# Optimization experiments

Hardware: AMD Instinct MI355X
Metric: run time of the kernel (lower is better)

Reference implementation:

```python
import jax, jax.numpy as jnp
import numpy as np

B, F, H, W = 1, 6, 20, 26
S = F * H * W            # 3120 tokens
DIM, NH, HD = 1536, 12, 128
C = HD // 2              # 64 rotary channels
T_C = C - 2 * (C // 3)   # 22 temporal channels
H_C = C // 3             # 21
W_C = C // 3             # 21
LOCAL_FRAMES = 4         # local_attn_size (in frames)
SINK_FRAMES = 1          # sink_size (in frames)
EPS = 1e-6
MAX_POS = 1024


def _angle_table(n_ch):
    inv = 1.0 / (10000.0 ** (np.arange(n_ch, dtype=np.float64) / n_ch))
    return np.outer(np.arange(MAX_POS, dtype=np.float64), inv)


def setup_inputs() -> dict:
    key = jax.random.key(0)
    ks = jax.random.split(key, 8)
    sc = 0.02
    ang = np.concatenate([_angle_table(T_C), _angle_table(H_C), _angle_table(W_C)], axis=1)  # [1024, 64]
    return {
        "x": jax.random.normal(ks[0], (B, S, DIM), jnp.float32),
        "seq_lens": jnp.array([S], jnp.int32),
        "grid_sizes": jnp.array([[F, H, W]], jnp.int32),
        "freqs_cos": jnp.asarray(np.cos(ang), jnp.float32),
        "freqs_sin": jnp.asarray(np.sin(ang), jnp.float32),
        "Wq": jax.random.normal(ks[1], (DIM, DIM), jnp.float32) * sc,
        "bq": jnp.zeros((DIM,), jnp.float32),
        "Wk": jax.random.normal(ks[2], (DIM, DIM), jnp.float32) * sc,
        "bk": jnp.zeros((DIM,), jnp.float32),
        "Wv": jax.random.normal(ks[3], (DIM, DIM), jnp.float32) * sc,
        "bv": jnp.zeros((DIM,), jnp.float32),
        "Wo": jax.random.normal(ks[4], (DIM, DIM), jnp.float32) * sc,
        "bo": jnp.zeros((DIM,), jnp.float32),
        "gq": jnp.ones((DIM,), jnp.float32),
        "gk": jnp.ones((DIM,), jnp.float32),
    }


def _rms_norm(x, g):
    # WanRMSNorm: x * rsqrt(mean(x^2) + eps) * weight
    return x * jax.lax.rsqrt(jnp.mean(x * x, axis=-1, keepdims=True) + EPS) * g


def _rope_apply(x, freqs_cos, freqs_sin):
    # x: [B, S, NH, HD]; per-token 3D (f,h,w) rotary on consecutive pairs.
    pos = jnp.arange(S)
    f = pos // (H * W)
    hh = (pos // W) % H
    ww = pos % W
    cos_t, cos_h, cos_w = freqs_cos[:, :T_C], freqs_cos[:, T_C:T_C + H_C], freqs_cos[:, T_C + H_C:]
    sin_t, sin_h, sin_w = freqs_sin[:, :T_C], freqs_sin[:, T_C:T_C + H_C], freqs_sin[:, T_C + H_C:]
    cos = jnp.concatenate([cos_t[f], cos_h[hh], cos_w[ww]], axis=-1)[None, :, None, :]  # [1,S,1,C]
    sin = jnp.concatenate([sin_t[f], sin_h[hh], sin_w[ww]], axis=-1)[None, :, None, :]
    xp = x.reshape(B, S, NH, C, 2)
    xr, xi = xp[..., 0], xp[..., 1]
    out = jnp.stack([xr * cos - xi * sin, xr * sin + xi * cos], axis=-1)
    return out.reshape(B, S, NH, HD)


def _block_mask():
    # frame-causal + local window (in frames) + sink frames: [S, S] bool
    fid = jnp.arange(S) // (H * W)
    fi, fj = fid[:, None], fid[None, :]
    return (fj <= fi) & ((fi - fj < LOCAL_FRAMES) | (fj < SINK_FRAMES))


def reference(x, seq_lens, grid_sizes, freqs_cos, freqs_sin,
              Wq, bq, Wk, bk, Wv, bv, Wo, bo, gq, gk):
    q = _rms_norm(x @ Wq + bq, gq).reshape(B, S, NH, HD)
    k = _rms_norm(x @ Wk + bk, gk).reshape(B, S, NH, HD)
    v = (x @ Wv + bv).reshape(B, S, NH, HD)
    rq = _rope_apply(q, freqs_cos, freqs_sin)
    rk = _rope_apply(k, freqs_cos, freqs_sin)
    scale = 1.0 / jnp.sqrt(jnp.asarray(HD, x.dtype))
    scores = jnp.einsum('bind,bjnd->bnij', rq, rk) * scale  # [B,NH,S,S]
    scores = jnp.where(_block_mask()[None, None], scores, jnp.finfo(scores.dtype).min)
    attn = jax.nn.softmax(scores, axis=-1)
    out = jnp.einsum('bnij,bjnd->bind', attn, v).reshape(B, S, DIM)
    return out @ Wo + bo
```

## Files before the change

kernel.cpp:

```cpp
#include <hip/hip_runtime.h>
#include <hip/hip_bf16.h>
#include <stdint.h>

typedef short v8s __attribute__((ext_vector_type(8)));
typedef float v4f __attribute__((ext_vector_type(4)));
typedef unsigned short u16;

#define S_LEN 3120
#define DIMN 1536
#define NHEAD 12
#define HDIM 128
#define FRM 520
#define NT64 49
#define T64_PH 166
#define TOT64 1992
#define NSTEP32 17
#define SCALE_QK 0.088388347648318447f
#define MAXOFF 12.0f

struct TaskMap {
  unsigned char tile[T64_PH];
  unsigned char frame[T64_PH];
  short accv[NT64];
  unsigned char nf[NT64];
};
constexpr TaskMap make_map() {
  TaskMap m{};
  int acc = 0;
  for (int tile = 0; tile < NT64; ++tile) {
    int q0t = tile * 64;
    int f_lo = q0t / FRM;
    int qhi = q0t + 63 < S_LEN - 1 ? q0t + 63 : S_LEN - 1;
    int f_hi = qhi / FRM;
    int fstart = f_lo - 3 > 0 ? f_lo - 3 : 0;
    int sink = fstart > 0 ? 1 : 0;
    int nf = f_hi - fstart + 1 + sink;
    m.accv[tile] = (short)acc;
    m.nf[tile] = (unsigned char)nf;
    for (int c = 0; c < nf; ++c) {
      m.tile[acc + c] = (unsigned char)tile;
      m.frame[acc + c] = (unsigned char)(sink ? (c == 0 ? 0 : fstart + c - 1) : (fstart + c));
    }
    acc += nf;
  }
  return m;
}
__device__ __constant__ TaskMap TM = make_map();

__device__ __forceinline__ v4f mfma16(v8s a, v8s b, v4f c) {
  return __builtin_amdgcn_mfma_f32_16x16x32_bf16(a, b, c, 0, 0, 0);
}
__device__ __forceinline__ float b2f(u16 u) {
  union { float f; unsigned int i; } x; x.i = ((unsigned int)u) << 16; return x.f;
}
__device__ __forceinline__ u16 f2b(float f) {
  union { float f; unsigned int i; } x; x.f = f;
  unsigned int r = x.i + 0x7FFFu + ((x.i >> 16) & 1u);
  return (u16)(r >> 16);
}
__device__ __forceinline__ void async16(const void* g, void* l) {
  __builtin_amdgcn_global_load_lds(
      (__attribute__((address_space(1))) const void*)g,
      (__attribute__((address_space(3))) void*)l, 16, 0, 0);
}

__global__ void detect_dtype(const u16* __restrict__ w, int* __restrict__ flag) {
  __shared__ int sh;
  int t = threadIdx.x;
  if (t == 0) sh = 0;
  __syncthreads();
  u16 m0 = (u16)(w[2 * t] & 0x7FFF);
  u16 m1 = (u16)(w[2 * t + 1] & 0x7FFF);
  if (m0 >= 0x4480 || m1 >= 0x4480) atomicOr(&sh, 1);
  __syncthreads();
  if (t == 0) *flag = sh;
}

struct PrepArgs {
  const void* tin[4]; u16* tout[4];
  const void* csrc[9]; u16* cdst[9]; int cn[9];
};
__global__ __launch_bounds__(256) void prep(PrepArgs a, const int* __restrict__ flag) {
  int isf = *flag;
  int z = blockIdx.z;
  int t = threadIdx.x;
  if (z < 4) {
    __shared__ u16 tile[32][33];
    const float* inf = (const float*)a.tin[z];
    const u16* inb = (const u16*)a.tin[z];
    u16* out = a.tout[z];
    int tx = t & 31, ty = t >> 5;
    int gr0 = blockIdx.y * 32, gc0 = blockIdx.x * 32;
#pragma unroll
    for (int i = 0; i < 4; ++i) {
      int r = ty + i * 8;
      size_t idx = (size_t)(gr0 + r) * DIMN + gc0 + tx;
      tile[r][tx] = isf ? f2b(inf[idx]) : inb[idx];
    }
    __syncthreads();
#pragma unroll
    for (int i = 0; i < 4; ++i) {
      int r = ty + i * 8;
      out[(size_t)(gc0 + r) * DIMN + gr0 + tx] = tile[tx][r];
    }
  } else {
    int id = z - 4;
    int n = a.cn[id];
    const float* sf = (const float*)a.csrc[id];
    const u16* sb = (const u16*)a.csrc[id];
    u16* d = a.cdst[id];
    int bidx = blockIdx.y * gridDim.x + blockIdx.x;
    int stride = gridDim.x * gridDim.y * 256;
    for (int i = bidx * 256 + t; i < n; i += stride)
      d[i] = isf ? f2b(sf[i]) : sb[i];
  }
}

__global__ __launch_bounds__(256) void transpose16(const u16* __restrict__ in,
                                                   u16* __restrict__ out,
                                                   int rows, int cols) {
  __shared__ u16 tile[32][33];
  int t = threadIdx.x;
  int tx = t & 31, ty = t >> 5;
  int gr0 = blockIdx.y * 32, gc0 = blockIdx.x * 32;
#pragma unroll
  for (int i = 0; i < 4; ++i) {
    int r = ty + i * 8;
    int gr = gr0 + r, gc = gc0 + tx;
    if (gr < rows && gc < cols) tile[r][tx] = in[(size_t)gr * cols + gc];
  }
  __syncthreads();
#pragma unroll
  for (int i = 0; i < 4; ++i) {
    int r = ty + i * 8;
    int orow = gc0 + r, ocol = gr0 + tx;
    if (orow < cols && ocol < rows) out[(size_t)orow * rows + ocol] = tile[tx][r];
  }
}

template <int MT, int NT>
__global__ __launch_bounds__(256) void gemm3(
    const u16* __restrict__ A,
    const u16* BT0, const u16* BT1, const u16* BT2,
    const u16* b0, const u16* b1, const u16* b2,
    void* C0, void* C1, void* C2, int M, const int* __restrict__ flag, int dyn) {
  static_assert(MT == 64, "4-wave layout assumes MT==64");
  const u16* BT; const u16* bias; void* C;
  if (blockIdx.z == 0)      { BT = BT0; bias = b0; C = C0; }
  else if (blockIdx.z == 1) { BT = BT1; bias = b1; C = C1; }
  else                      { BT = BT2; bias = b2; C = C2; }
  int f32out = dyn ? *flag : 0;
  __shared__ __align__(16) short As[MT * 64];
  __shared__ __align__(16) short Bs[NT * 64];
  int t = threadIdx.x, w = t >> 6, l = t & 63;
  int ln = l & 15, lg = l >> 4;
  int m0 = blockIdx.y * MT, n0 = blockIdx.x * NT;
  int lr = l >> 3;
  int gl = (l & 7) ^ lr;
  constexpr int ACH = MT / 32;
  constexpr int BCH = NT / 32;
  const u16* gAp[ACH]; short* lAp[ACH];
#pragma unroll
  for (int i = 0; i < ACH; ++i) {
    int c = w * ACH + i;
    int arow = min(m0 + c * 8 + lr, M - 1);
    gAp[i] = A + (size_t)arow * DIMN + gl * 8;
    lAp[i] = As + c * 512;
  }
  const u16* gBp[BCH]; short* lBp[BCH];
#pragma unroll
  for (int i = 0; i < BCH; ++i) {
    int c = w * BCH + i;
    int brow = n0 + c * 8 + lr;
    gBp[i] = BT + (size_t)brow * DIMN + gl * 8;
    lBp[i] = Bs + c * 512;
  }
  constexpr int NJ = NT / 64;
  int aoff[2][4], boff[2][NJ];
#pragma unroll
  for (int ks = 0; ks < 2; ++ks) {
#pragma unroll
    for (int i = 0; i < 4; ++i) {
      int ar = i * 16 + ln;
      aoff[ks][i] = ar * 64 + (((ks * 4 + lg) ^ (ar & 7)) * 8);
    }
#pragma unroll
    for (int j = 0; j < NJ; ++j) {
      int br = w * (NJ * 16) + j * 16 + ln;
      boff[ks][j] = br * 64 + (((ks * 4 + lg) ^ (br & 7)) * 8);
    }
  }
  v4f acc[4][NJ] = {};
  for (int k0 = 0; k0 < DIMN; k0 += 64) {
    __syncthreads();
#pragma unroll
    for (int i = 0; i < ACH; ++i) async16(gAp[i] + k0, lAp[i]);
#pragma unroll
    for (int i = 0; i < BCH; ++i) async16(gBp[i] + k0, lBp[i]);
    __syncthreads();
#pragma unroll
    for (int ks = 0; ks < 2; ++ks) {
      v8s af[4], bfr[NJ];
#pragma unroll
      for (int i = 0; i < 4; ++i) af[i] = *(const v8s*)(As + aoff[ks][i]);
#pragma unroll
      for (int j = 0; j < NJ; ++j) bfr[j] = *(const v8s*)(Bs + boff[ks][j]);
#pragma unroll
      for (int i = 0; i < 4; ++i)
#pragma unroll
        for (int j = 0; j < NJ; ++j) acc[i][j] = mfma16(af[i], bfr[j], acc[i][j]);
    }
  }
#pragma unroll
  for (int i = 0; i < 4; ++i) {
    int rb = m0 + i * 16 + lg * 4;
#pragma unroll
    for (int j = 0; j < NJ; ++j) {
      int col = n0 + w * (NJ * 16) + j * 16 + ln;
      float bv = b2f(bias[col]);
#pragma unroll
      for (int r = 0; r < 4; ++r) {
        int grow = rb + r;
        if (grow < M) {
          size_t idx = (size_t)grow * DIMN + col;
          float val = acc[i][j][r] + bv;
          if (f32out) ((float*)C)[idx] = val;
          else        ((u16*)C)[idx] = f2b(val);
        }
      }
    }
  }
}

__global__ __launch_bounds__(256) void norm_rope(u16* __restrict__ Q, u16* __restrict__ K,
                                                 const u16* __restrict__ gq,
                                                 const u16* __restrict__ gk,
                                                 const u16* __restrict__ fcos,
                                                 const u16* __restrict__ fsin) {
  int s = blockIdx.x;
  u16* base = (blockIdx.y == 0 ? Q : K) + (size_t)s * DIMN;
  const u16* g = (blockIdx.y == 0) ? gq : gk;
  int t = threadIdx.x;
  int e = t * 6;
  float x[6];
#pragma unroll
  for (int i = 0; i < 6; ++i) x[i] = b2f(base[e + i]);
  float ss = 0.f;
#pragma unroll
  for (int i = 0; i < 6; ++i) ss += x[i] * x[i];
#pragma unroll
  for (int off = 32; off > 0; off >>= 1) ss += __shfl_xor(ss, off);
  __shared__ float red[4];
  if ((t & 63) == 0) red[t >> 6] = ss;
  __syncthreads();
  float tot = red[0] + red[1] + red[2] + red[3];
  float rs = rsqrtf(tot * (1.0f / DIMN) + 1e-6f);
  int f = s / FRM;
  int hh = (s / 26) % 20;
  int ww = s % 26;
#pragma unroll
  for (int u = 0; u < 3; ++u) {
    int e0 = e + 2 * u;
    int c = (e0 & 127) >> 1;
    int p = (c < 22) ? f : ((c < 43) ? hh : ww);
    float co = b2f(fcos[p * 64 + c]);
    float si = b2f(fsin[p * 64 + c]);
    float xr = x[2 * u] * rs * b2f(g[e0]);
    float xi = x[2 * u + 1] * rs * b2f(g[e0 + 1]);
    base[e0]     = f2b(xr * co - xi * si);
    base[e0 + 1] = f2b(xr * si + xi * co);
  }
}

__global__ __launch_bounds__(128) void attn_block(const u16* __restrict__ Q,
                                                  const u16* __restrict__ K,
                                                  const u16* __restrict__ VT,
                                                  u16* __restrict__ Po,
                                                  float* __restrict__ Pl) {
  __shared__ __align__(16) short Ks[2][32 * 128];
  __shared__ __align__(16) short Vs[2][128 * 32];
  __shared__ __align__(16) short Pt[2][32 * 40];
  int t = threadIdx.x, w = t >> 6, l = t & 63;
  int ln = l & 15, lg = l >> 4;
  int task = blockIdx.x;
  int head = task / T64_PH, tid = task % T64_PH;
  int tile = TM.tile[tid], frame = TM.frame[tid];
  int q0 = tile * 64 + w * 32;
  v8s qf[2][4];
  bool rowok[2][4];
#pragma unroll
  for (int g = 0; g < 2; ++g) {
    int row = min(q0 + g * 16 + ln, S_LEN - 1);
    const u16* qp = Q + (size_t)row * DIMN + head * HDIM + lg * 8;
#pragma unroll
    for (int c = 0; c < 4; ++c) qf[g][c] = *(const v8s*)(qp + c * 32);
#pragma unroll
    for (int r = 0; r < 4; ++r) {
      int qr = q0 + g * 16 + lg * 4 + r;
      int fi = (qr < S_LEN) ? qr / FRM : -1;
      rowok[g][r] = (frame <= fi) && ((fi - frame) < 4 || frame == 0);
    }
  }
  float lsum[2][4] = {};
  v4f o[2][8] = {};
  int kbeg = frame * FRM, kend = kbeg + FRM;
  int kr_i[4], kgl_i[4], vd_i[4], vgl_i[4];
#pragma unroll
  for (int i = 0; i < 4; ++i) {
    int n = (w * 4 + i) * 64 + l;
    kr_i[i] = n >> 4;
    kgl_i[i] = (n & 15) ^ (kr_i[i] & 15);
    vd_i[i] = n >> 2;
    vgl_i[i] = (n & 3) ^ (vd_i[i] & 3);
  }
  const u16* Kb = K + head * HDIM;
  {
    int kb = kbeg;
#pragma unroll
    for (int i = 0; i < 4; ++i) {
      int krow = min(kb + kr_i[i], S_LEN - 1);
      async16(Kb + (size_t)krow * DIMN + kgl_i[i] * 8,
              (char*)Ks + (size_t)(w * 4 + i) * 1024);
      async16(VT + (size_t)(head * HDIM + vd_i[i]) * S_LEN + kb + vgl_i[i] * 8,
              (char*)Vs + (size_t)(w * 4 + i) * 1024);
    }
  }
  __syncthreads();
  for (int it = 0; it < NSTEP32; ++it) {
    int cur = it & 1;
    if (it + 1 < NSTEP32) {
      int kbn = kbeg + (it + 1) * 32;
      size_t boff = (size_t)(cur ^ 1) * 8192;
#pragma unroll
      for (int i = 0; i < 4; ++i) {
        int krow = min(kbn + kr_i[i], S_LEN - 1);
        async16(Kb + (size_t)krow * DIMN + kgl_i[i] * 8,
                (char*)Ks + boff + (size_t)(w * 4 + i) * 1024);
        async16(VT + (size_t)(head * HDIM + vd_i[i]) * S_LEN + kbn + vgl_i[i] * 8,
                (char*)Vs + boff + (size_t)(w * 4 + i) * 1024);
      }
    }
    int kb = kbeg + it * 32;
    v4f s[2][2] = {};
    __builtin_amdgcn_s_setprio(1);
#pragma unroll
    for (int kg = 0; kg < 2; ++kg) {
#pragma unroll
      for (int c = 0; c < 4; ++c) {
        v8s kf = *(const v8s*)(&Ks[cur][(kg * 16 + ln) * 128 + (((c * 4 + lg) ^ ln) * 8)]);
        s[0][kg] = mfma16(qf[0][c], kf, s[0][kg]);
        s[1][kg] = mfma16(qf[1][c], kf, s[1][kg]);
      }
    }
    __builtin_amdgcn_s_setprio(0);
#pragma unroll
    for (int g = 0; g < 2; ++g)
#pragma unroll
      for (int kg = 0; kg < 2; ++kg) {
        bool jv = (kb + kg * 16 + ln) < kend;
#pragma unroll
        for (int r = 0; r < 4; ++r) {
          float p = (rowok[g][r] && jv) ? __expf(s[g][kg][r] * SCALE_QK - MAXOFF) : 0.f;
          unsigned int bi = __float_as_uint(p) & 0xffff0000u;
          lsum[g][r] += __uint_as_float(bi);
          Pt[w][(g * 16 + lg * 4 + r) * 40 + kg * 16 + ln] = (u16)(bi >> 16);
        }
      }
    v8s pf0 = *(const v8s*)(&Pt[w][ln * 40 + lg * 8]);
    v8s pf1 = *(const v8s*)(&Pt[w][(16 + ln) * 40 + lg * 8]);
    __builtin_amdgcn_s_setprio(1);
#pragma unroll
    for (int d = 0; d < 8; ++d) {
      int rr = d * 16 + ln;
      v8s vf = *(const v8s*)(&Vs[cur][rr * 32 + ((lg ^ (rr & 3)) * 8)]);
      o[0][d] = mfma16(pf0, vf, o[0][d]);
      o[1][d] = mfma16(pf1, vf, o[1][d]);
    }
    __builtin_amdgcn_s_setprio(0);
    __syncthreads();
  }
#pragma unroll
  for (int g = 0; g < 2; ++g)
#pragma unroll
    for (int r = 0; r < 4; ++r) {
      float v = lsum[g][r];
      v += __shfl_xor(v, 1);
      v += __shfl_xor(v, 2);
      v += __shfl_xor(v, 4);
      v += __shfl_xor(v, 8);
      lsum[g][r] = v;
    }
  size_t pbase = (size_t)task * (64 * 128);
#pragma unroll
  for (int g = 0; g < 2; ++g)
#pragma unroll
    for (int d = 0; d < 8; ++d)
#pragma unroll
      for (int r = 0; r < 4; ++r) {
        int lrow = w * 32 + g * 16 + lg * 4 + r;
        Po[pbase + lrow * 128 + d * 16 + ln] = f2b(o[g][d][r]);
      }
  if (ln == 0) {
#pragma unroll
    for (int g = 0; g < 2; ++g)
#pragma unroll
      for (int r = 0; r < 4; ++r)
        Pl[task * 64 + w * 32 + g * 16 + lg * 4 + r] = lsum[g][r];
  }
}

__global__ __launch_bounds__(256) void attn_combine(const u16* __restrict__ Po,
                                                    const float* __restrict__ Pl,
                                                    u16* __restrict__ Oa) {
  int tile = blockIdx.x, h = blockIdx.y;
  int accv = TM.accv[tile], nf = TM.nf[tile];
  int base = h * T64_PH + accv;
  int t = threadIdx.x;
  int row = t >> 2, seg = (t & 3) * 32;
  int grow = tile * 64 + row;
  if (grow >= S_LEN) return;
  float lsum = 0.f;
  float ao[32];
#pragma unroll
  for (int j = 0; j < 32; ++j) ao[j] = 0.f;
  for (int c = 0; c < nf; ++c) {
    int task = base + c;
    lsum += Pl[task * 64 + row];
    const u16* p = Po + (size_t)task * 8192 + row * 128 + seg;
#pragma unroll
    for (int v = 0; v < 4; ++v) {
      v8s x = *(const v8s*)(p + v * 8);
#pragma unroll
      for (int j = 0; j < 8; ++j) ao[v * 8 + j] += b2f((u16)x[j]);
    }
  }
  float inv = 1.0f / lsum;
  u16* dst = Oa + (size_t)grow * DIMN + h * HDIM + seg;
#pragma unroll
  for (int v = 0; v < 4; ++v) {
    v8s res;
#pragma unroll
    for (int j = 0; j < 8; ++j) res[j] = (short)f2b(ao[v * 8 + j] * inv);
    *(v8s*)(dst + v * 8) = res;
  }
}

extern "C" void kernel_launch(void* const* d_in, const int* in_sizes, int n_in,
                              void* d_out, int out_size, void* d_ws, size_t ws_size,
                              hipStream_t stream) {
  (void)n_in; (void)out_size; (void)ws_size;
  int* flag = (int*)d_ws;
  u16* ws = (u16*)d_ws;
  size_t off = 16;
  const size_t SD = (size_t)S_LEN * DIMN;
  const size_t WW = (size_t)DIMN * DIMN;
  const size_t NPO = (size_t)1032 * 128 * 128;
  auto alloc = [&](size_t n) { u16* p = ws + off; off += (n + 7) & ~(size_t)7; return p; };
  u16* Xc  = alloc(SD);
  u16* Fc  = alloc(65536);
  u16* Fs  = alloc(65536);
  u16* bqc = alloc(1536); u16* bkc = alloc(1536); u16* bvc = alloc(1536); u16* boc = alloc(1536);
  u16* gqc = alloc(1536); u16* gkc = alloc(1536);
  u16* Qr = alloc(SD); u16* Kr = alloc(SD); u16* Vr = alloc(SD); u16* Oa = alloc(SD);
  u16* WoT = alloc(WW);
  u16* WqT = alloc(WW); u16* WkT = alloc(WW); u16* WvT = alloc(WW);
  alloc(NPO - 3 * WW);
  float* Pl = (float*)alloc((size_t)TOT64 * 64 * 2);
  u16* Po = WqT;
  u16* VT = Xc;

  detect_dtype<<<1, 256, 0, stream>>>((const u16*)d_in[5], flag);

  PrepArgs pa;
  pa.tin[0] = d_in[5];  pa.tout[0] = WqT;
  pa.tin[1] = d_in[7];  pa.tout[1] = WkT;
  pa.tin[2] = d_in[9];  pa.tout[2] = WvT;
  pa.tin[3] = d_in[11]; pa.tout[3] = WoT;
  const int srcIdx[9] = {0, 3, 4, 6, 8, 10, 12, 13, 14};
  u16* dsts[9] = {Xc, Fc, Fs, bqc, bkc, bvc, boc, gqc, gkc};
  for (int i = 0; i < 9; ++i) {
    pa.csrc[i] = d_in[srcIdx[i]];
    pa.cdst[i] = dsts[i];
    pa.cn[i] = in_sizes[srcIdx[i]];
  }
  dim3 b256(256);
  prep<<<dim3(48, 48, 13), b256, 0, stream>>>(pa, flag);
  gemm3<64, 256><<<dim3(6, 49, 3), b256, 0, stream>>>(Xc, WqT, WkT, WvT, bqc, bkc, bvc,
                                                      Qr, Kr, Vr, S_LEN, flag, 0);
  norm_rope<<<dim3(S_LEN, 2), b256, 0, stream>>>(Qr, Kr, gqc, gkc, Fc, Fs);
  transpose16<<<dim3(48, 98), b256, 0, stream>>>(Vr, VT, S_LEN, DIMN);
  attn_block<<<dim3(TOT64), dim3(128), 0, stream>>>(Qr, Kr, VT, Po, Pl);
  attn_combine<<<dim3(NT64, NHEAD), b256, 0, stream>>>(Po, Pl, Oa);
  gemm3<64, 256><<<dim3(6, 49, 1), b256, 0, stream>>>(Oa, WoT, WoT, WoT, boc, boc, boc,
                                                      d_out, d_out, d_out, S_LEN, flag, 1);
}
```

Before: 381.5 us.

## Fuse V transpose into QKV GEMM epilogue, vectorize prep and norm_rope, shrink GEMM tiles

```diff
diff --git a/kernel.cpp b/kernel.cpp
--- a/kernel.cpp
+++ b/kernel.cpp
@@ -3,6 +3,7 @@
 #include <stdint.h>
 
 typedef short v8s __attribute__((ext_vector_type(8)));
+typedef short v4h __attribute__((ext_vector_type(4)));
 typedef float v4f __attribute__((ext_vector_type(4)));
 typedef unsigned short u16;
 
@@ -84,57 +85,42 @@
   int isf = *flag;
   int z = blockIdx.z;
   int t = threadIdx.x;
+  int bidx = blockIdx.y * gridDim.x + blockIdx.x;
   if (z < 4) {
-    __shared__ u16 tile[32][33];
     const float* inf = (const float*)a.tin[z];
     const u16* inb = (const u16*)a.tin[z];
     u16* out = a.tout[z];
-    int tx = t & 31, ty = t >> 5;
-    int gr0 = blockIdx.y * 32, gc0 = blockIdx.x * 32;
-#pragma unroll
-    for (int i = 0; i < 4; ++i) {
-      int r = ty + i * 8;
-      size_t idx = (size_t)(gr0 + r) * DIMN + gc0 + tx;
-      tile[r][tx] = isf ? f2b(inf[idx]) : inb[idx];
-    }
-    __syncthreads();
-#pragma unroll
-    for (int i = 0; i < 4; ++i) {
-      int r = ty + i * 8;
-      out[(size_t)(gc0 + r) * DIMN + gr0 + tx] = tile[tx][r];
-    }
+    int row = (bidx % 24) * 64 + (t & 63);
+    int c0 = (bidx / 24) * 16 + (t >> 6) * 4;
+    float v[4];
+    if (isf) {
+      float4 d = *(const float4*)(inf + (size_t)row * DIMN + c0);
+      v[0] = d.x; v[1] = d.y; v[2] = d.z; v[3] = d.w;
+    } else {
+      ushort4 d = *(const ushort4*)(inb + (size_t)row * DIMN + c0);
+      v[0] = b2f(d.x); v[1] = b2f(d.y); v[2] = b2f(d.z); v[3] = b2f(d.w);
+    }
+#pragma unroll
+    for (int k = 0; k < 4; ++k)
+      out[(size_t)(c0 + k) * DIMN + row] = f2b(v[k]);
   } else {
     int id = z - 4;
-    int n = a.cn[id];
+    int n4 = a.cn[id] >> 2;
     const float* sf = (const float*)a.csrc[id];
     const u16* sb = (const u16*)a.csrc[id];
     u16* d = a.cdst[id];
-    int bidx = blockIdx.y * gridDim.x + blockIdx.x;
     int stride = gridDim.x * gridDim.y * 256;
-    for (int i = bidx * 256 + t; i < n; i += stride)
-      d[i] = isf ? f2b(sf[i]) : sb[i];
-  }
-}
-
-__global__ __launch_bounds__(256) void transpose16(const u16* __restrict__ in,
-                                                   u16* __restrict__ out,
-                                                   int rows, int cols) {
-  __shared__ u16 tile[32][33];
-  int t = threadIdx.x;
-  int tx = t & 31, ty = t >> 5;
-  int gr0 = blockIdx.y * 32, gc0 = blockIdx.x * 32;
-#pragma unroll
-  for (int i = 0; i < 4; ++i) {
-    int r = ty + i * 8;
-    int gr = gr0 + r, gc = gc0 + tx;
-    if (gr < rows && gc < cols) tile[r][tx] = in[(size_t)gr * cols + gc];
-  }
-  __syncthreads();
-#pragma unroll
-  for (int i = 0; i < 4; ++i) {
-    int r = ty + i * 8;
-    int orow = gc0 + r, ocol = gr0 + tx;
-    if (orow < cols && ocol < rows) out[(size_t)orow * rows + ocol] = tile[tx][r];
+    for (int i = bidx * 256 + t; i < n4; i += stride) {
+      v4h o;
+      if (isf) {
+        float4 x4 = *(const float4*)(sf + (size_t)i * 4);
+        o[0] = (short)f2b(x4.x); o[1] = (short)f2b(x4.y);
+        o[2] = (short)f2b(x4.z); o[3] = (short)f2b(x4.w);
+      } else {
+        o = *(const v4h*)(sb + (size_t)i * 4);
+      }
+      *(v4h*)(d + (size_t)i * 4) = o;
+    }
   }
 }
 
@@ -211,6 +197,23 @@
         for (int j = 0; j < NJ; ++j) acc[i][j] = mfma16(af[i], bfr[j], acc[i][j]);
     }
   }
+  if ((!dyn) && blockIdx.z == 2) {
+#pragma unroll
+    for (int i = 0; i < 4; ++i) {
+      int rb = m0 + i * 16 + lg * 4;
+      if (rb + 3 >= M) continue;
+#pragma unroll
+      for (int j = 0; j < NJ; ++j) {
+        int col = n0 + w * (NJ * 16) + j * 16 + ln;
+        float bv = b2f(bias[col]);
+        v4h pk;
+#pragma unroll
+        for (int r = 0; r < 4; ++r) pk[r] = (short)f2b(acc[i][j][r] + bv);
+        *(v4h*)((u16*)C + (size_t)col * S_LEN + rb) = pk;
+      }
+    }
+    return;
+  }
 #pragma unroll
   for (int i = 0; i < 4; ++i) {
     int rb = m0 + i * 16 + lg * 4;
@@ -237,38 +240,48 @@
                                                  const u16* __restrict__ gk,
                                                  const u16* __restrict__ fcos,
                                                  const u16* __restrict__ fsin) {
-  int s = blockIdx.x;
+  int t = threadIdx.x, w = t >> 6, l = t & 63;
+  int s = blockIdx.x * 4 + w;
   u16* base = (blockIdx.y == 0 ? Q : K) + (size_t)s * DIMN;
   const u16* g = (blockIdx.y == 0) ? gq : gk;
-  int t = threadIdx.x;
-  int e = t * 6;
-  float x[6];
-#pragma unroll
-  for (int i = 0; i < 6; ++i) x[i] = b2f(base[e + i]);
+  v8s xv[3], gv[3];
+#pragma unroll
+  for (int c = 0; c < 3; ++c) {
+    xv[c] = *(const v8s*)(base + c * 512 + l * 8);
+    gv[c] = *(const v8s*)(g + c * 512 + l * 8);
+  }
+  float x[24];
   float ss = 0.f;
 #pragma unroll
-  for (int i = 0; i < 6; ++i) ss += x[i] * x[i];
+  for (int c = 0; c < 3; ++c)
+#pragma unroll
+    for (int j = 0; j < 8; ++j) {
+      float v = b2f((u16)xv[c][j]);
+      x[c * 8 + j] = v;
+      ss += v * v;
+    }
 #pragma unroll
   for (int off = 32; off > 0; off >>= 1) ss += __shfl_xor(ss, off);
-  __shared__ float red[4];
-  if ((t & 63) == 0) red[t >> 6] = ss;
-  __syncthreads();
-  float tot = red[0] + red[1] + red[2] + red[3];
-  float rs = rsqrtf(tot * (1.0f / DIMN) + 1e-6f);
+  float rs = rsqrtf(ss * (1.0f / DIMN) + 1e-6f);
   int f = s / FRM;
   int hh = (s / 26) % 20;
   int ww = s % 26;
 #pragma unroll
-  for (int u = 0; u < 3; ++u) {
-    int e0 = e + 2 * u;
-    int c = (e0 & 127) >> 1;
-    int p = (c < 22) ? f : ((c < 43) ? hh : ww);
-    float co = b2f(fcos[p * 64 + c]);
-    float si = b2f(fsin[p * 64 + c]);
-    float xr = x[2 * u] * rs * b2f(g[e0]);
-    float xi = x[2 * u + 1] * rs * b2f(g[e0 + 1]);
-    base[e0]     = f2b(xr * co - xi * si);
-    base[e0 + 1] = f2b(xr * si + xi * co);
+  for (int c = 0; c < 3; ++c) {
+    v8s out;
+#pragma unroll
+    for (int u = 0; u < 4; ++u) {
+      int e0 = c * 512 + l * 8 + 2 * u;
+      int ch = (e0 & 127) >> 1;
+      int p = (ch < 22) ? f : ((ch < 43) ? hh : ww);
+      float co = b2f(fcos[p * 64 + ch]);
+      float si = b2f(fsin[p * 64 + ch]);
+      float xr = x[c * 8 + 2 * u] * rs * b2f((u16)gv[c][2 * u]);
+      float xi = x[c * 8 + 2 * u + 1] * rs * b2f((u16)gv[c][2 * u + 1]);
+      out[2 * u]     = (short)f2b(xr * co - xi * si);
+      out[2 * u + 1] = (short)f2b(xr * si + xi * co);
+    }
+    *(v8s*)(base + c * 512 + l * 8) = out;
   }
 }
 
@@ -461,13 +474,14 @@
   u16* Fs  = alloc(65536);
   u16* bqc = alloc(1536); u16* bkc = alloc(1536); u16* bvc = alloc(1536); u16* boc = alloc(1536);
   u16* gqc = alloc(1536); u16* gkc = alloc(1536);
-  u16* Qr = alloc(SD); u16* Kr = alloc(SD); u16* Vr = alloc(SD); u16* Oa = alloc(SD);
+  u16* Qr = alloc(SD); u16* Kr = alloc(SD);
+  u16* VT = alloc(SD);
+  u16* Oa = alloc(SD);
   u16* WoT = alloc(WW);
   u16* WqT = alloc(WW); u16* WkT = alloc(WW); u16* WvT = alloc(WW);
   alloc(NPO - 3 * WW);
   float* Pl = (float*)alloc((size_t)TOT64 * 64 * 2);
   u16* Po = WqT;
-  u16* VT = Xc;
 
   detect_dtype<<<1, 256, 0, stream>>>((const u16*)d_in[5], flag);
 
@@ -485,12 +499,11 @@
   }
   dim3 b256(256);
   prep<<<dim3(48, 48, 13), b256, 0, stream>>>(pa, flag);
-  gemm3<64, 256><<<dim3(6, 49, 3), b256, 0, stream>>>(Xc, WqT, WkT, WvT, bqc, bkc, bvc,
-                                                      Qr, Kr, Vr, S_LEN, flag, 0);
-  norm_rope<<<dim3(S_LEN, 2), b256, 0, stream>>>(Qr, Kr, gqc, gkc, Fc, Fs);
-  transpose16<<<dim3(48, 98), b256, 0, stream>>>(Vr, VT, S_LEN, DIMN);
+  gemm3<64, 128><<<dim3(12, 49, 3), b256, 0, stream>>>(Xc, WqT, WkT, WvT, bqc, bkc, bvc,
+                                                       Qr, Kr, VT, S_LEN, flag, 0);
+  norm_rope<<<dim3(S_LEN / 4, 2), b256, 0, stream>>>(Qr, Kr, gqc, gkc, Fc, Fs);
   attn_block<<<dim3(TOT64), dim3(128), 0, stream>>>(Qr, Kr, VT, Po, Pl);
   attn_combine<<<dim3(NT64, NHEAD), b256, 0, stream>>>(Po, Pl, Oa);
-  gemm3<64, 256><<<dim3(6, 49, 1), b256, 0, stream>>>(Oa, WoT, WoT, WoT, boc, boc, boc,
-                                                      d_out, d_out, d_out, S_LEN, flag, 1);
-}
+  gemm3<64, 128><<<dim3(12, 49, 1), b256, 0, stream>>>(Oa, WoT, WoT, WoT, boc, boc, boc,
+                                                       d_out, d_out, d_out, S_LEN, flag, 1);
+}
```

New measurement: 349.3 us. 8.4% less time.
